# Performance work log

Hardware: AMD Instinct MI355X
Metric: run time of the kernel (lower is better)

Reference implementation:

```python
import jax, jax.numpy as jnp
from jax import lax
import numpy as np

B, T, H, L = 4096, 7, 512, 256
D = 2 * H  # bidirectional LSTM feature dim


def _lstm(x, wih, whh, bih, bhh, reverse):
    # x: [B, T, L]; torch gate order i, f, g, o
    b, hdim = x.shape[0], whh.shape[0]
    xs = jnp.swapaxes(x, 0, 1)  # [T, B, L]
    bias = bih + bhh

    def step(carry, xt):
        h, c = carry
        gates = xt @ wih + h @ whh + bias
        i, f, g, o = jnp.split(gates, 4, axis=-1)
        c = jax.nn.sigmoid(f) * c + jax.nn.sigmoid(i) * jnp.tanh(g)
        h = jax.nn.sigmoid(o) * jnp.tanh(c)
        return (h, c), h

    h0 = jnp.zeros((b, hdim), x.dtype)
    _, hs = lax.scan(step, (h0, h0), xs, reverse=reverse)
    return jnp.swapaxes(hs, 0, 1)  # [B, T, H]


def _att(enc, dec):
    # Sequential attention: keys/values start as enc and grow with each decoder output.
    keys = enc  # [B, T, D]
    outs = []
    for i in range(dec.shape[1]):  # fixed small T=7, Python loop is static
        q = dec[:, i, :]                                  # [B, D]
        scores = jnp.einsum('bd,btd->bt', q, keys)        # dot over features
        a = jax.nn.softmax(scores, axis=1)
        ctx = jnp.einsum('bt,btd->bd', a, keys)
        out = ctx + q
        outs.append(out)
        keys = jnp.concatenate([keys, out[:, None, :]], axis=1)
    return jnp.stack(outs, axis=1)  # [B, T, D]


def _deconv(x, w, b):
    # torch ConvTranspose2d (stride 1, pad 0) == full conv with flipped, in/out-swapped kernel
    kh, kw = w.shape[2], w.shape[3]
    w2 = jnp.transpose(w[:, :, ::-1, ::-1], (1, 0, 2, 3))  # [out, in, kh, kw]
    y = lax.conv_general_dilated(x, w2, (1, 1), ((kh - 1, kh - 1), (kw - 1, kw - 1)),
                                 dimension_numbers=('NCHW', 'OIHW', 'NCHW'))
    return y + b[None, :, None, None]


def setup_inputs() -> dict:
    key = jax.random.key(0)
    ks = jax.random.split(key, 12)
    p = lambda k, shape: jax.random.normal(k, shape, jnp.float32) * 0.02
    return {
        'lstm_enc': jax.random.normal(ks[0], (B, T, D), jnp.float32),
        'gaussian_noise': jax.random.normal(ks[1], (B, L), jnp.float32),
        'embedrep_w': p(ks[2], (L, L * T)), 'embedrep_b': jnp.zeros((L * T,), jnp.float32),
        'wih_f': p(ks[3], (L, 4 * H)), 'whh_f': p(ks[4], (H, 4 * H)),
        'bih_f': jnp.zeros((4 * H,), jnp.float32), 'bhh_f': jnp.zeros((4 * H,), jnp.float32),
        'wih_b': p(ks[5], (L, 4 * H)), 'whh_b': p(ks[6], (H, 4 * H)),
        'bih_b': jnp.zeros((4 * H,), jnp.float32), 'bhh_b': jnp.zeros((4 * H,), jnp.float32),
        'emb_w': p(ks[7], (D, 1024)), 'emb_b': jnp.zeros((1024,), jnp.float32),
        'dc3_w': p(ks[8], (64, 32, 1, 3)), 'dc3_b': jnp.zeros((32,), jnp.float32),
        'dc1_w': p(ks[9], (32, 16, 1, 5)), 'dc1_b': jnp.zeros((16,), jnp.float32),
        'dc2_w': p(ks[10], (16, 1, 3, 3)), 'dc2_b': jnp.zeros((1,), jnp.float32),
        'infer': 0,
    }


def reference(lstm_enc, gaussian_noise, embedrep_w, embedrep_b,
              wih_f, whh_f, bih_f, bhh_f, wih_b, whh_b, bih_b, bhh_b,
              emb_w, emb_b, dc3_w, dc3_b, dc1_w, dc1_b, dc2_w, dc2_b, infer):
    b = lstm_enc.shape[0]
    g1 = jax.nn.soft_sign(gaussian_noise @ embedrep_w + embedrep_b)   # [B, L*T]
    rep = g1.reshape(b, T, L)                                          # [B, 7, L]
    hf = _lstm(rep, wih_f, whh_f, bih_f, bhh_f, False)
    hb = _lstm(rep, wih_b, whh_b, bih_b, bhh_b, True)
    lstm1 = jnp.concatenate([hf, hb], axis=-1)                         # [B, 7, 2H]
    att_out = _att(lstm_enc, lstm1)                                    # [B, 7, 2H]
    emb = att_out @ emb_w + emb_b                                      # [B, 7, 1024]
    up = jax.nn.soft_sign(emb).reshape(b * T, 64, 1, 16)
    x = jax.nn.leaky_relu(_deconv(up, dc3_w, dc3_b))                   # [B*7, 32, 1, 18]
    x = jax.nn.leaky_relu(_deconv(x, dc1_w, dc1_b))                    # [B*7, 16, 1, 22]
    x = jax.nn.leaky_relu(_deconv(x, dc2_w, dc2_b))                    # [B*7, 1, 3, 24]
    x = jax.nn.softmax(x, axis=2)                                      # softmax over H dim (=3)
    out = x.reshape(b, T, 1, 3, 24)[:, :, -1, :, :]                    # [B, 7, 3, 24]
    return out
```

## Files before the change

kernel.cpp:

```cpp
#include <hip/hip_runtime.h>
#include <stdint.h>


typedef __attribute__((ext_vector_type(4))) float f32x4;
typedef __attribute__((ext_vector_type(8))) short bf16x8;
typedef __attribute__((ext_vector_type(4))) unsigned short us4;

__device__ __forceinline__ unsigned short f2b(float f) {
  union { float f; unsigned u; } x; x.f = f;
  unsigned r = x.u + 0x7FFFu + ((x.u >> 16) & 1u);
  return (unsigned short)(r >> 16);
}
__device__ __forceinline__ float b2f(unsigned short s) {
  union { unsigned u; float f; } x; x.u = ((unsigned)s) << 16; return x.f;
}
__device__ __forceinline__ float sigmoidf(float x) {
  return 1.f / (1.f + __expf(-x));
}
__device__ __forceinline__ float fast_tanh(float x) {
  x = fminf(15.f, fmaxf(-15.f, x));
  float e = __expf(2.f * x);
  return (e - 1.f) / (e + 1.f);
}

__device__ __forceinline__ void gl_lds16(const void* g, void* l) {
  auto gp = reinterpret_cast<const __attribute__((address_space(1))) unsigned int*>(
      reinterpret_cast<uintptr_t>(g));
  auto lp = reinterpret_cast<__attribute__((address_space(3))) unsigned int*>(
      reinterpret_cast<uintptr_t>(l));
  __builtin_amdgcn_global_load_lds(gp, lp, 16, 0, 0);
}


__device__ __forceinline__ void stage_half(const unsigned short* src, int ld,
                                           unsigned short* hbase, int tid) {
  const int row_in = tid >> 2;
  const int gidx = tid & 3;
#pragma unroll
  for (int r = 0; r < 2; ++r) {
    int row = r * 128 + row_in;
    int gsrc = gidx ^ ((row >> 1) & 3);
    gl_lds16(src + (size_t)row * ld + gsrc * 8, hbase + r * 4096 + (tid >> 6) * 512);
  }
}

__device__ __forceinline__ bf16x8 lds_fragH(const unsigned short* hbase, int row, int lq) {
  return *(const bf16x8*)(hbase + row * 32 + (lq ^ (((row >> 1) & 3) << 3)));
}

template <int N>
__device__ __forceinline__ void gate() {
  if constexpr (N == 8) asm volatile("s_waitcnt vmcnt(8)" ::: "memory");
  else if constexpr (N == 4) asm volatile("s_waitcnt vmcnt(4)" ::: "memory");
  else asm volatile("s_waitcnt vmcnt(0)" ::: "memory");
}

#define TILE_TOP(N)                     \
  gate<N>();                            \
  __builtin_amdgcn_s_barrier();         \
  __builtin_amdgcn_sched_barrier(0)

template <class FA, class FB>
__device__ __forceinline__ void tile32(const unsigned short* Ab, const unsigned short* Bb,
                                       int wm, int wn, int lane, f32x4 (&acc)[8][4],
                                       FA stageA, FB stageB) {
  const int lr = lane & 15, lq = (lane >> 4) * 8;
  bf16x8 a[8], b[4];
#pragma unroll
  for (int i = 0; i < 4; ++i) a[i] = lds_fragH(Ab, wm * 128 + i * 16 + lr, lq);
#pragma unroll
  for (int n = 0; n < 4; ++n) b[n] = lds_fragH(Bb, wn * 64 + n * 16 + lr, lq);
  __builtin_amdgcn_sched_barrier(0);
#pragma unroll
  for (int i = 4; i < 8; ++i) a[i] = lds_fragH(Ab, wm * 128 + i * 16 + lr, lq);
  stageA();
  asm volatile("s_waitcnt lgkmcnt(4)" ::: "memory");
  __builtin_amdgcn_sched_barrier(0);
  __builtin_amdgcn_s_setprio(1);
#pragma unroll
  for (int i = 0; i < 4; ++i)
#pragma unroll
    for (int n = 0; n < 4; ++n)
      acc[i][n] = __builtin_amdgcn_mfma_f32_16x16x32_bf16(a[i], b[n], acc[i][n], 0, 0, 0);
  __builtin_amdgcn_s_setprio(0);
  stageB();
  asm volatile("s_waitcnt lgkmcnt(0)" ::: "memory");
  __builtin_amdgcn_sched_barrier(0);
  __builtin_amdgcn_s_setprio(1);
#pragma unroll
  for (int i = 4; i < 8; ++i)
#pragma unroll
    for (int n = 0; n < 4; ++n)
      acc[i][n] = __builtin_amdgcn_mfma_f32_16x16x32_bf16(a[i], b[n], acc[i][n], 0, 0, 0);
  __builtin_amdgcn_s_setprio(0);
}

__device__ __forceinline__ void stage128x64(const unsigned short* src, int ld,
                                            unsigned short* lds, int wv, int lane) {
#pragma unroll
  for (int r = 0; r < 4; ++r) {
    int row = r * 32 + wv * 8 + (lane >> 3);
    gl_lds16(src + (size_t)row * ld + (lane & 7) * 8, lds + (r * 32 + wv * 8) * 64);
  }
}
__device__ __forceinline__ void mfma_tile(const unsigned short* As, const unsigned short* Bs,
                                          int wm, int wn, int lane, f32x4 acc[4][4]) {
#pragma unroll
  for (int kk = 0; kk < 2; ++kk) {
    int ko = kk * 32 + (lane >> 4) * 8;
    bf16x8 a[4], b[4];
#pragma unroll
    for (int i = 0; i < 4; ++i)
      a[i] = *(const bf16x8*)(As + (size_t)(wm * 64 + i * 16 + (lane & 15)) * 64 + ko);
#pragma unroll
    for (int i = 0; i < 4; ++i)
      b[i] = *(const bf16x8*)(Bs + (size_t)(wn * 64 + i * 16 + (lane & 15)) * 64 + ko);
#pragma unroll
    for (int mi = 0; mi < 4; ++mi)
#pragma unroll
      for (int ni = 0; ni < 4; ++ni)
        acc[mi][ni] = __builtin_amdgcn_mfma_f32_16x16x32_bf16(a[mi], b[ni], acc[mi][ni], 0, 0, 0);
  }
}

__global__ __launch_bounds__(256) void pack_kernel(
    const float* __restrict__ noise, const float* __restrict__ erep_w,
    const float* __restrict__ emb_w,
    const float* __restrict__ wih_f, const float* __restrict__ whh_f,
    const float* __restrict__ bih_f, const float* __restrict__ bhh_f,
    const float* __restrict__ wih_b, const float* __restrict__ whh_b,
    const float* __restrict__ bih_b, const float* __restrict__ bhh_b,
    unsigned short* __restrict__ noiseb, unsigned short* __restrict__ erepT,
    unsigned short* __restrict__ embT, unsigned short* __restrict__ lstmW,
    float* __restrict__ lstmB) {
  const int N0 = 4096 * 256;
  const int N1 = 1792 * 256;
  const int N2 = 1024 * 1024;
  const int N3 = 2 * 2048 * 768;
  const int N4 = 2 * 2048;
  const int total = N0 + N1 + N2 + N3 + N4;
  for (int i = blockIdx.x * 256 + threadIdx.x; i < total; i += gridDim.x * 256) {
    int x = i;
    if (x < N0) { noiseb[x] = f2b(noise[x]); continue; }
    x -= N0;
    if (x < N1) { int n = x >> 8, k = x & 255; erepT[x] = f2b(erep_w[k * 1792 + n]); continue; }
    x -= N1;
    if (x < N2) {
      int n = x >> 10, k = x & 1023;
      int o = (n & 63) * 16 + (n >> 6);
      embT[x] = f2b(emb_w[k * 1024 + o]);
      continue;
    }
    x -= N2;
    if (x < N3) {
      int dir = x / (2048 * 768);
      int r = x - dir * (2048 * 768);
      int npk = r / 768, k = r - (r / 768) * 768;
      int blk = npk >> 6, g = (npk >> 4) & 3, u = npk & 15;
      int o = g * 512 + blk * 16 + u;
      const float* wih = dir ? wih_b : wih_f;
      const float* whh = dir ? whh_b : whh_f;
      float v = (k < 256) ? wih[k * 2048 + o] : whh[(k - 256) * 2048 + o];
      lstmW[x] = f2b(v);
      continue;
    }
    x -= N3;
    {
      int dir = x >> 11, npk = x & 2047;
      int blk = npk >> 6, g = (npk >> 4) & 3, u = npk & 15;
      int o = g * 512 + blk * 16 + u;
      lstmB[x] = dir ? (bih_b[o] + bhh_b[o]) : (bih_f[o] + bhh_f[o]);
    }
  }
}

__global__ __launch_bounds__(256) void gemm_rep_kernel(
    const unsigned short* __restrict__ A, const unsigned short* __restrict__ Bt,
    const float* __restrict__ bias, unsigned short* __restrict__ rep_t) {
  __shared__ unsigned short As[128 * 64];
  __shared__ unsigned short Bs[128 * 64];
  const int lane = threadIdx.x & 63, wv = threadIdx.x >> 6;
  const int wm = wv >> 1, wn = wv & 1;
  const int m0 = blockIdx.y * 128, n0 = blockIdx.x * 128;
  f32x4 acc[4][4];
#pragma unroll
  for (int i = 0; i < 4; ++i)
#pragma unroll
    for (int j = 0; j < 4; ++j) acc[i][j] = (f32x4){0.f, 0.f, 0.f, 0.f};
  for (int k0 = 0; k0 < 256; k0 += 64) {
    stage128x64(A + (size_t)m0 * 256 + k0, 256, As, wv, lane);
    stage128x64(Bt + (size_t)n0 * 256 + k0, 256, Bs, wv, lane);
    __syncthreads();
    mfma_tile(As, Bs, wm, wn, lane, acc);
    __syncthreads();
  }
#pragma unroll
  for (int ni = 0; ni < 4; ++ni) {
    int n = n0 + wn * 64 + ni * 16 + (lane & 15);
    float bv = bias[n];
    int t = n >> 8, l = n & 255;
#pragma unroll
    for (int mi = 0; mi < 4; ++mi)
#pragma unroll
      for (int r = 0; r < 4; ++r) {
        int m = m0 + wm * 64 + mi * 16 + (lane >> 4) * 4 + r;
        float v = acc[mi][ni][r] + bv;
        v = v / (1.f + fabsf(v));
        rep_t[((size_t)t * 4096 + m) * 256 + l] = f2b(v);
      }
  }
}

__global__ __launch_bounds__(512, 2) void lstm_step256_kernel(
    const unsigned short* __restrict__ rep_t, const unsigned short* __restrict__ Wp,
    const float* __restrict__ biasP, unsigned short* __restrict__ hbuf,
    float* __restrict__ cbuf, unsigned short* __restrict__ lstm1, int step) {
  __shared__ unsigned short Ar[4][8192];
  __shared__ unsigned short Br[4][8192];
  const int tid = threadIdx.x, lane = tid & 63, wv = tid >> 6;
  const int wm = wv >> 2, wn = wv & 3;
  const int swz = (blockIdx.x & 7) * 32 + (blockIdx.x >> 3);
  const int dir = swz >> 7;
  const int by = (swz & 127) >> 3, bx = swz & 7;
  const int m0 = by * 256, n0 = bx * 256;
  const int t_proc = dir ? (6 - step) : step;
  const unsigned short* W = Wp + (size_t)dir * 2048 * 768;
  const unsigned short* hin = hbuf + ((size_t)(step & 1) * 2 + dir) * (4096 * 512);
  unsigned short* hout = hbuf + ((size_t)((step + 1) & 1) * 2 + dir) * (4096 * 512);
  float* cp = cbuf + (size_t)dir * (4096 * 512);
  const unsigned short* xsrc = rep_t + (size_t)t_proc * 4096 * 256;

  f32x4 acc[8][4];
#pragma unroll
  for (int i = 0; i < 8; ++i)
#pragma unroll
    for (int j = 0; j < 4; ++j) acc[i][j] = (f32x4){0.f, 0.f, 0.f, 0.f};

  auto asrc = [&](int tt) {
    return tt < 8 ? xsrc + (size_t)m0 * 256 + tt * 32
                  : hin + (size_t)m0 * 512 + (tt - 8) * 32;
  };
  auto ald = [&](int tt) { return tt < 8 ? 256 : 512; };

  stage_half(asrc(0), ald(0), Ar[0], tid);
  stage_half(W + (size_t)n0 * 768 + 0 * 32, 768, Br[0], tid);
  stage_half(asrc(1), ald(1), Ar[1], tid);
  stage_half(W + (size_t)n0 * 768 + 1 * 32, 768, Br[1], tid);
  stage_half(asrc(2), ald(2), Ar[2], tid);
  stage_half(W + (size_t)n0 * 768 + 2 * 32, 768, Br[2], tid);

  for (int t = 0; t <= 20; ++t) {
    TILE_TOP(8);
    const int tt = t + 3;
    tile32(Ar[t & 3], Br[t & 3], wm, wn, lane, acc,
           [&] { stage_half(asrc(tt), ald(tt), Ar[tt & 3], tid); },
           [&] { stage_half(W + (size_t)n0 * 768 + tt * 32, 768, Br[tt & 3], tid); });
  }
  TILE_TOP(8);
  tile32(Ar[21 & 3], Br[21 & 3], wm, wn, lane, acc, [&] {}, [&] {});
  TILE_TOP(4);
  tile32(Ar[22 & 3], Br[22 & 3], wm, wn, lane, acc, [&] {}, [&] {});
  TILE_TOP(0);
  tile32(Ar[23 & 3], Br[23 & 3], wm, wn, lane, acc, [&] {}, [&] {});

  const int u = lane & 15;
  const int blk = (n0 + wn * 64) >> 6;
  const int j = blk * 16 + u;
  const float bz0 = biasP[dir * 2048 + blk * 64 + 0 * 16 + u];
  const float bz1 = biasP[dir * 2048 + blk * 64 + 1 * 16 + u];
  const float bz2 = biasP[dir * 2048 + blk * 64 + 2 * 16 + u];
  const float bz3 = biasP[dir * 2048 + blk * 64 + 3 * 16 + u];
#pragma unroll
  for (int mi = 0; mi < 8; ++mi)
#pragma unroll
    for (int r = 0; r < 4; ++r) {
      int row = m0 + wm * 128 + mi * 16 + (lane >> 4) * 4 + r;
      float gi = acc[mi][0][r] + bz0;
      float gf = acc[mi][1][r] + bz1;
      float gg = acc[mi][2][r] + bz2;
      float go = acc[mi][3][r] + bz3;
      size_t ci = (size_t)row * 512 + j;
      float c = sigmoidf(gf) * cp[ci] + sigmoidf(gi) * fast_tanh(gg);
      cp[ci] = c;
      float h = sigmoidf(go) * fast_tanh(c);
      unsigned short hb = f2b(h);
      hout[ci] = hb;
      lstm1[((size_t)row * 7 + t_proc) * 1024 + dir * 512 + j] = hb;
    }
}

__global__ __launch_bounds__(256) void att_fused2_kernel(
    const float* __restrict__ enc, const unsigned short* __restrict__ lstm1,
    unsigned short* __restrict__ att) {
  __shared__ unsigned short Qs[7 * 1032];
  __shared__ unsigned short Ehs[7 * 1032];
  __shared__ unsigned short Els[7 * 1032];
  __shared__ float P[4 * 2 * 64 * 4];
  __shared__ float sG[98];
  __shared__ float sC[7][14];
  __shared__ float sA[16];
  const int tid = threadIdx.x, lane = tid & 63, wv = tid >> 6;
  const int b = blockIdx.x;
  const float* Eb = enc + (size_t)b * 7168;
  const unsigned short* Qb = lstm1 + (size_t)b * 7168;

  if (tid < 98) ((float*)sC)[tid] = 0.f;

  const f32x4* Eb4 = (const f32x4*)Eb;
#pragma unroll
  for (int r = 0; r < 7; ++r) {
    f32x4 v = Eb4[r * 256 + tid];
    us4 hi, lo;
#pragma unroll
    for (int e = 0; e < 4; ++e) {
      hi[e] = f2b(v[e]);
      lo[e] = f2b(v[e] - b2f(hi[e]));
    }
    *(us4*)&Ehs[r * 1032 + tid * 4] = hi;
    *(us4*)&Els[r * 1032 + tid * 4] = lo;
  }
  const bf16x8* Qb8 = (const bf16x8*)Qb;
#pragma unroll
  for (int r = 0; r < 4; ++r) {
    int idx = r * 256 + tid;
    if (idx < 896) {
      int row = idx >> 7, col = (idx & 127) * 8;
      *(bf16x8*)&Qs[row * 1032 + col] = Qb8[idx];
    }
  }
  __syncthreads();

  {
    const int rr = lane & 15;
    const int rowc = rr > 6 ? 6 : rr;
    const int kbase = wv * 256 + (lane >> 4) * 8;
    f32x4 g1 = {0.f, 0.f, 0.f, 0.f}, g2 = {0.f, 0.f, 0.f, 0.f};
#pragma unroll
    for (int s = 0; s < 8; ++s) {
      const int k0 = kbase + s * 32;
      bf16x8 aq = *(const bf16x8*)&Qs[rowc * 1032 + k0];
      bf16x8 bh = *(const bf16x8*)&Ehs[rowc * 1032 + k0];
      bf16x8 bl = *(const bf16x8*)&Els[rowc * 1032 + k0];
      g1 = __builtin_amdgcn_mfma_f32_16x16x32_bf16(aq, bh, g1, 0, 0, 0);
      g1 = __builtin_amdgcn_mfma_f32_16x16x32_bf16(aq, bl, g1, 0, 0, 0);
      g2 = __builtin_amdgcn_mfma_f32_16x16x32_bf16(aq, aq, g2, 0, 0, 0);
    }
    *(f32x4*)&P[((wv * 2 + 0) * 64 + lane) * 4] = g1;
    *(f32x4*)&P[((wv * 2 + 1) * 64 + lane) * 4] = g2;
  }
  __syncthreads();

  if (tid < 98) {
    int i = tid / 14, v = tid - i * 14;
    int col = v < 7 ? v : v - 7;
    int tile = v < 7 ? 0 : 1;
    int ln = ((i >> 2) << 4) | col;
    int rg = i & 3;
    float s = 0.f;
#pragma unroll
    for (int w = 0; w < 4; ++w) s += P[((w * 2 + tile) * 64 + ln) * 4 + rg];
    sG[i * 14 + v] = s;
  }
  __syncthreads();

  if (wv == 0) {
    for (int i = 0; i < 7; ++i) {
      const int nt = 7 + i;
      float s = -1e30f;
      if (lane < 7) {
        s = sG[i * 14 + lane];
      } else if (lane < nt) {
        int jj = lane - 7;
        float a2 = 0.f;
#pragma unroll
        for (int v = 0; v < 14; ++v) a2 += sC[jj][v] * sG[i * 14 + v];
        s = a2;
      }
      float mx = s;
#pragma unroll
      for (int off = 8; off >= 1; off >>= 1) mx = fmaxf(mx, __shfl_xor(mx, off, 16));
      float e = (lane < nt) ? __expf(s - mx) : 0.f;
      float sum = e;
#pragma unroll
      for (int off = 8; off >= 1; off >>= 1) sum += __shfl_xor(sum, off, 16);
      float a = e / sum;
      if (lane < 16) sA[lane] = a;
      if (lane < 14) {
        float c = (lane < 7) ? sA[lane] : 0.f;
        for (int jj = 0; jj < i; ++jj) c += sA[7 + jj] * sC[jj][lane];
        if (lane == 7 + i) c += 1.f;
        sC[i][lane] = c;
      }
    }
  }
  __syncthreads();

  {
    const int d0 = tid * 4;
    float acc[7][4];
#pragma unroll
    for (int i = 0; i < 7; ++i)
#pragma unroll
      for (int e = 0; e < 4; ++e) acc[i][e] = 0.f;
#pragma unroll
    for (int t = 0; t < 7; ++t) {
      us4 h = *(const us4*)&Ehs[t * 1032 + d0];
      us4 l = *(const us4*)&Els[t * 1032 + d0];
      float ev[4];
#pragma unroll
      for (int e = 0; e < 4; ++e) ev[e] = b2f(h[e]) + b2f(l[e]);
#pragma unroll
      for (int i = 0; i < 7; ++i) {
        float c = sC[i][t];
#pragma unroll
        for (int e = 0; e < 4; ++e) acc[i][e] += c * ev[e];
      }
    }
#pragma unroll
    for (int m = 0; m < 7; ++m) {
      us4 qv = *(const us4*)&Qs[m * 1032 + d0];
      float qf[4];
#pragma unroll
      for (int e = 0; e < 4; ++e) qf[e] = b2f(qv[e]);
#pragma unroll
      for (int i = m; i < 7; ++i) {
        float c = sC[i][7 + m];
#pragma unroll
        for (int e = 0; e < 4; ++e) acc[i][e] += c * qf[e];
      }
    }
    unsigned short* Ab = att + (size_t)b * 7168;
#pragma unroll
    for (int i = 0; i < 7; ++i) {
      us4 r;
#pragma unroll
      for (int e = 0; e < 4; ++e) r[e] = f2b(acc[i][e]);
      *(us4*)(Ab + i * 1024 + d0) = r;
    }
  }
}

__global__ __launch_bounds__(512, 2) void gemm_emb256_kernel(
    const unsigned short* __restrict__ A, const unsigned short* __restrict__ Bt,
    const float* __restrict__ bias, unsigned short* __restrict__ up_t) {
  __shared__ unsigned short Ar[4][8192];
  __shared__ unsigned short Br[4][8192];
  const int tid = threadIdx.x, lane = tid & 63, wv = tid >> 6;
  const int wm = wv >> 2, wn = wv & 3;
  const int swz = (blockIdx.x & 7) * 56 + (blockIdx.x >> 3);
  const int by = swz >> 2, bx = swz & 3;
  const int m0 = by * 256, n0 = bx * 256;

  f32x4 acc[8][4];
#pragma unroll
  for (int i = 0; i < 8; ++i)
#pragma unroll
    for (int j = 0; j < 4; ++j) acc[i][j] = (f32x4){0.f, 0.f, 0.f, 0.f};

  const unsigned short* Abase = A + (size_t)m0 * 1024;
  const unsigned short* Bbase = Bt + (size_t)n0 * 1024;

  stage_half(Abase + 0 * 32, 1024, Ar[0], tid);
  stage_half(Bbase + 0 * 32, 1024, Br[0], tid);
  stage_half(Abase + 1 * 32, 1024, Ar[1], tid);
  stage_half(Bbase + 1 * 32, 1024, Br[1], tid);
  stage_half(Abase + 2 * 32, 1024, Ar[2], tid);
  stage_half(Bbase + 2 * 32, 1024, Br[2], tid);

  for (int t = 0; t <= 28; ++t) {
    TILE_TOP(8);
    const int tt = t + 3;
    tile32(Ar[t & 3], Br[t & 3], wm, wn, lane, acc,
           [&] { stage_half(Abase + tt * 32, 1024, Ar[tt & 3], tid); },
           [&] { stage_half(Bbase + tt * 32, 1024, Br[tt & 3], tid); });
  }
  TILE_TOP(8);
  tile32(Ar[29 & 3], Br[29 & 3], wm, wn, lane, acc, [&] {}, [&] {});
  TILE_TOP(4);
  tile32(Ar[30 & 3], Br[30 & 3], wm, wn, lane, acc, [&] {}, [&] {});
  TILE_TOP(0);
  tile32(Ar[31 & 3], Br[31 & 3], wm, wn, lane, acc, [&] {}, [&] {});

#pragma unroll
  for (int ni = 0; ni < 4; ++ni) {
    int np = n0 + wn * 64 + ni * 16 + (lane & 15);
    int o = (np & 63) * 16 + (np >> 6);
    float bv = bias[o];
#pragma unroll
    for (int mi = 0; mi < 8; ++mi)
#pragma unroll
      for (int r = 0; r < 4; ++r) {
        int m = m0 + wm * 128 + mi * 16 + (lane >> 4) * 4 + r;
        float v = acc[mi][ni][r] + bv;
        v = v / (1.f + fabsf(v));
        up_t[(size_t)m * 1024 + np] = f2b(v);
      }
  }
}

__global__ __launch_bounds__(256) void dc3_kernel(const unsigned short* __restrict__ up_t,
                                                  const float* __restrict__ w3,
                                                  const float* __restrict__ b3,
                                                  unsigned short* __restrict__ y1_t) {
  const int lane = threadIdx.x & 63, wv = threadIdx.x >> 6;
  const int kq = (lane >> 4) * 8;
  const int oc = lane & 15;
  bf16x8 bf[2][6];
#pragma unroll
  for (int nt = 0; nt < 2; ++nt)
#pragma unroll
    for (int kk = 0; kk < 6; ++kk) {
      bf16x8 v;
#pragma unroll
      for (int t = 0; t < 8; ++t) {
        int k = kk * 32 + kq + t;
        int jj = k >> 6, ic = k & 63;
        v[t] = (short)f2b(w3[((size_t)ic * 32 + nt * 16 + oc) * 3 + jj]);
      }
      bf[nt][kk] = v;
    }
  const float bia0 = b3[oc], bia1 = b3[16 + oc];
  const int base_chunk = blockIdx.x * 32 + wv * 8;
  for (int cc = 0; cc < 8; ++cc) {
    const int chunk = base_chunk + cc;
    int m = chunk * 16 + (lane & 15);
    int img = m / 18, ow = m - img * 18;
    const unsigned short* arow = up_t + (size_t)img * 1024;
    f32x4 acc0 = {0.f, 0.f, 0.f, 0.f}, acc1 = {0.f, 0.f, 0.f, 0.f};
#pragma unroll
    for (int kk = 0; kk < 6; ++kk) {
      int jj = kk >> 1;
      int ic0 = (kk & 1) * 32 + kq;
      int iw = ow - jj;
      bf16x8 a = {0, 0, 0, 0, 0, 0, 0, 0};
      if ((unsigned)iw < 16u) a = *(const bf16x8*)(arow + iw * 64 + ic0);
      acc0 = __builtin_amdgcn_mfma_f32_16x16x32_bf16(a, bf[0][kk], acc0, 0, 0, 0);
      acc1 = __builtin_amdgcn_mfma_f32_16x16x32_bf16(a, bf[1][kk], acc1, 0, 0, 0);
    }
#pragma unroll
    for (int r = 0; r < 4; ++r) {
      int mm = chunk * 16 + (lane >> 4) * 4 + r;
      float v0 = acc0[r] + bia0; v0 = v0 > 0.f ? v0 : 0.01f * v0;
      float v1 = acc1[r] + bia1; v1 = v1 > 0.f ? v1 : 0.01f * v1;
      y1_t[(size_t)mm * 32 + oc] = f2b(v0);
      y1_t[(size_t)mm * 32 + 16 + oc] = f2b(v1);
    }
  }
}

__global__ __launch_bounds__(256) void dc1_kernel(const unsigned short* __restrict__ y1_t,
                                                  const float* __restrict__ w1,
                                                  const float* __restrict__ b1,
                                                  unsigned short* __restrict__ y2_t) {
  const int lane = threadIdx.x & 63, wv = threadIdx.x >> 6;
  const int kq = (lane >> 4) * 8;
  const int oc = lane & 15;
  bf16x8 bf[5];
#pragma unroll
  for (int kk = 0; kk < 5; ++kk) {
    bf16x8 v;
#pragma unroll
    for (int t = 0; t < 8; ++t) {
      int ic = kq + t;
      v[t] = (short)f2b(w1[((size_t)ic * 16 + oc) * 5 + kk]);
    }
    bf[kk] = v;
  }
  const float bia = b1[oc];
  const int base_chunk = blockIdx.x * 32 + wv * 8;
  for (int cc = 0; cc < 8; ++cc) {
    const int chunk = base_chunk + cc;
    int m = chunk * 16 + (lane & 15);
    int img = m / 22, ow = m - img * 22;
    const unsigned short* abase = y1_t + (size_t)img * 18 * 32;
    f32x4 acc = {0.f, 0.f, 0.f, 0.f};
#pragma unroll
    for (int kk = 0; kk < 5; ++kk) {
      int iw = ow - kk;
      bf16x8 a = {0, 0, 0, 0, 0, 0, 0, 0};
      if ((unsigned)iw < 18u) a = *(const bf16x8*)(abase + iw * 32 + kq);
      acc = __builtin_amdgcn_mfma_f32_16x16x32_bf16(a, bf[kk], acc, 0, 0, 0);
    }
#pragma unroll
    for (int r = 0; r < 4; ++r) {
      int mm = chunk * 16 + (lane >> 4) * 4 + r;
      float v = acc[r] + bia;
      v = v > 0.f ? v : 0.01f * v;
      y2_t[(size_t)mm * 16 + oc] = f2b(v);
    }
  }
}

__global__ __launch_bounds__(256) void dc2_kernel(const unsigned short* __restrict__ y2_t,
                                                  const float* __restrict__ w2,
                                                  const float* __restrict__ b2,
                                                  float* __restrict__ out) {
  int idx = blockIdx.x * 256 + threadIdx.x;
  int img = idx / 24, ow = idx - img * 24;
  float lg0 = b2[0], lg1 = b2[0], lg2 = b2[0];
#pragma unroll
  for (int jj = 0; jj < 3; ++jj) {
    int iw = ow - jj;
    if ((unsigned)iw >= 22u) continue;
    const unsigned short* row = y2_t + ((size_t)img * 22 + iw) * 16;
    bf16x8 v0 = *(const bf16x8*)(row);
    bf16x8 v1 = *(const bf16x8*)(row + 8);
    float x[16];
#pragma unroll
    for (int ic = 0; ic < 8; ++ic) {
      x[ic] = b2f((unsigned short)v0[ic]);
      x[8 + ic] = b2f((unsigned short)v1[ic]);
    }
#pragma unroll
    for (int ic = 0; ic < 16; ++ic) {
      lg0 += x[ic] * w2[ic * 9 + 0 * 3 + jj];
      lg1 += x[ic] * w2[ic * 9 + 1 * 3 + jj];
      lg2 += x[ic] * w2[ic * 9 + 2 * 3 + jj];
    }
  }
  lg0 = lg0 > 0.f ? lg0 : 0.01f * lg0;
  lg1 = lg1 > 0.f ? lg1 : 0.01f * lg1;
  lg2 = lg2 > 0.f ? lg2 : 0.01f * lg2;
  float mx = fmaxf(lg0, fmaxf(lg1, lg2));
  float e0 = __expf(lg0 - mx), e1 = __expf(lg1 - mx), e2 = __expf(lg2 - mx);
  float inv = 1.f / (e0 + e1 + e2);
  size_t ob = (size_t)img * 72 + ow;
  out[ob] = e0 * inv;
  out[ob + 24] = e1 * inv;
  out[ob + 48] = e2 * inv;
}

extern "C" void kernel_launch(void* const* d_in, const int* in_sizes, int n_in,
                              void* d_out, int out_size, void* d_ws, size_t ws_size,
                              hipStream_t stream) {
  (void)in_sizes; (void)n_in; (void)out_size; (void)ws_size;
  const float* enc    = (const float*)d_in[0];
  const float* noise  = (const float*)d_in[1];
  const float* erep_w = (const float*)d_in[2];
  const float* erep_b = (const float*)d_in[3];
  const float* wih_f  = (const float*)d_in[4];
  const float* whh_f  = (const float*)d_in[5];
  const float* bih_f  = (const float*)d_in[6];
  const float* bhh_f  = (const float*)d_in[7];
  const float* wih_b  = (const float*)d_in[8];
  const float* whh_b  = (const float*)d_in[9];
  const float* bih_b  = (const float*)d_in[10];
  const float* bhh_b  = (const float*)d_in[11];
  const float* emb_w  = (const float*)d_in[12];
  const float* emb_b  = (const float*)d_in[13];
  const float* dc3w   = (const float*)d_in[14];
  const float* dc3b   = (const float*)d_in[15];
  const float* dc1w   = (const float*)d_in[16];
  const float* dc1b   = (const float*)d_in[17];
  const float* dc2w   = (const float*)d_in[18];
  const float* dc2b   = (const float*)d_in[19];
  float* out = (float*)d_out;

  char* p = (char*)d_ws;
  auto carve = [&p](size_t bytes) {
    char* r = p;
    p += (bytes + 255) & ~(size_t)255;
    return r;
  };
  unsigned short* rep_t  = (unsigned short*)carve(7ull * 4096 * 256 * 2);
  unsigned short* lstmW  = (unsigned short*)carve(2ull * 2048 * 768 * 2);
  float*          lstmB  = (float*)carve(2ull * 2048 * 4);
  unsigned short* noiseb = (unsigned short*)carve(4096ull * 256 * 2);
  unsigned short* erepT  = (unsigned short*)carve(1792ull * 256 * 2);
  unsigned short* embT   = (unsigned short*)carve(1024ull * 1024 * 2);
  unsigned short* hbuf   = (unsigned short*)carve(4ull * 4096 * 512 * 2);
  float*          cbuf   = (float*)carve(2ull * 4096 * 512 * 4);
  unsigned short* lstm1  = (unsigned short*)carve(4096ull * 7 * 1024 * 2);
  unsigned short* att    = (unsigned short*)carve(28672ull * 1024 * 2);
  unsigned short* up_t   = (unsigned short*)carve(28672ull * 1024 * 2);
  unsigned short* y1_t   = (unsigned short*)carve(28672ull * 18 * 32 * 2);
  unsigned short* y2_t   = (unsigned short*)carve(28672ull * 22 * 16 * 2);

  hipMemsetAsync(hbuf, 0, 2ull * 4096 * 512 * 2, stream);
  hipMemsetAsync(cbuf, 0, 2ull * 4096 * 512 * 4, stream);

  pack_kernel<<<2048, 256, 0, stream>>>(noise, erep_w, emb_w, wih_f, whh_f, bih_f, bhh_f,
                                        wih_b, whh_b, bih_b, bhh_b,
                                        noiseb, erepT, embT, lstmW, lstmB);
  gemm_rep_kernel<<<dim3(14, 32), 256, 0, stream>>>(noiseb, erepT, erep_b, rep_t);
  for (int s = 0; s < 7; ++s)
    lstm_step256_kernel<<<256, 512, 0, stream>>>(rep_t, lstmW, lstmB, hbuf, cbuf, lstm1, s);
  att_fused2_kernel<<<4096, 256, 0, stream>>>(enc, lstm1, att);
  gemm_emb256_kernel<<<448, 512, 0, stream>>>(att, embT, emb_b, up_t);
  dc3_kernel<<<1008, 256, 0, stream>>>(up_t, dc3w, dc3b, y1_t);
  dc1_kernel<<<1232, 256, 0, stream>>>(y1_t, dc1w, dc1b, y2_t);
  dc2_kernel<<<2688, 256, 0, stream>>>(y2_t, dc2w, dc2b, out);
}
```

Measured before the change: 510.0 us.

## Restructure GEMM pipelines, store LSTM cell state in bf16, drop split-bf16 attention

The LDS-ring GEMM loop in the LSTM-step and embedding kernels now prefetches the next tile's fragments into registers while the current MFMAs run, replacing the split half-tile staging. The LSTM cell state buffer moves from fp32 to bf16, halving its read/write traffic per step. The attention kernel drops the hi/lo bf16 split of the encoder, using a single bf16 copy, and replaces a block barrier with an LDS waitcnt. These trade numerical precision for fewer MFMAs and less memory traffic, and the cell state rounding accumulates across steps.

```diff
diff --git a/kernel.cpp b/kernel.cpp
--- a/kernel.cpp
+++ b/kernel.cpp
@@ -48,52 +48,33 @@
   return *(const bf16x8*)(hbase + row * 32 + (lq ^ (((row >> 1) & 3) << 3)));
 }
 
-template <int N>
-__device__ __forceinline__ void gate() {
-  if constexpr (N == 8) asm volatile("s_waitcnt vmcnt(8)" ::: "memory");
-  else if constexpr (N == 4) asm volatile("s_waitcnt vmcnt(4)" ::: "memory");
-  else asm volatile("s_waitcnt vmcnt(0)" ::: "memory");
-}
-
-#define TILE_TOP(N)                     \
-  gate<N>();                            \
-  __builtin_amdgcn_s_barrier();         \
-  __builtin_amdgcn_sched_barrier(0)
-
-template <class FA, class FB>
-__device__ __forceinline__ void tile32(const unsigned short* Ab, const unsigned short* Bb,
-                                       int wm, int wn, int lane, f32x4 (&acc)[8][4],
-                                       FA stageA, FB stageB) {
+__device__ __forceinline__ void tile_reads(const unsigned short* Ab, const unsigned short* Bb,
+                                           int wm, int wn, int lane,
+                                           bf16x8 (&a)[8], bf16x8 (&b)[4]) {
   const int lr = lane & 15, lq = (lane >> 4) * 8;
-  bf16x8 a[8], b[4];
-#pragma unroll
-  for (int i = 0; i < 4; ++i) a[i] = lds_fragH(Ab, wm * 128 + i * 16 + lr, lq);
+#pragma unroll
+  for (int i = 0; i < 8; ++i) a[i] = lds_fragH(Ab, wm * 128 + i * 16 + lr, lq);
 #pragma unroll
   for (int n = 0; n < 4; ++n) b[n] = lds_fragH(Bb, wn * 64 + n * 16 + lr, lq);
-  __builtin_amdgcn_sched_barrier(0);
-#pragma unroll
-  for (int i = 4; i < 8; ++i) a[i] = lds_fragH(Ab, wm * 128 + i * 16 + lr, lq);
-  stageA();
-  asm volatile("s_waitcnt lgkmcnt(4)" ::: "memory");
-  __builtin_amdgcn_sched_barrier(0);
+}
+
+__device__ __forceinline__ void tile_mfma(bf16x8 (&a)[8], bf16x8 (&b)[4], f32x4 (&acc)[8][4]) {
   __builtin_amdgcn_s_setprio(1);
 #pragma unroll
-  for (int i = 0; i < 4; ++i)
+  for (int i = 0; i < 8; ++i)
 #pragma unroll
     for (int n = 0; n < 4; ++n)
       acc[i][n] = __builtin_amdgcn_mfma_f32_16x16x32_bf16(a[i], b[n], acc[i][n], 0, 0, 0);
   __builtin_amdgcn_s_setprio(0);
-  stageB();
-  asm volatile("s_waitcnt lgkmcnt(0)" ::: "memory");
+}
+
+#define RING_TOP(t, NT)                                                   \
+  if ((t) < (NT)-2) asm volatile("s_waitcnt vmcnt(4)" ::: "memory");      \
+  else              asm volatile("s_waitcnt vmcnt(0)" ::: "memory");      \
+  __builtin_amdgcn_s_barrier();                                           \
+  __builtin_amdgcn_sched_barrier(0);                                      \
+  asm volatile("s_waitcnt lgkmcnt(0)" ::: "memory");                      \
   __builtin_amdgcn_sched_barrier(0);
-  __builtin_amdgcn_s_setprio(1);
-#pragma unroll
-  for (int i = 4; i < 8; ++i)
-#pragma unroll
-    for (int n = 0; n < 4; ++n)
-      acc[i][n] = __builtin_amdgcn_mfma_f32_16x16x32_bf16(a[i], b[n], acc[i][n], 0, 0, 0);
-  __builtin_amdgcn_s_setprio(0);
-}
 
 __device__ __forceinline__ void stage128x64(const unsigned short* src, int ld,
                                             unsigned short* lds, int wv, int lane) {
@@ -214,7 +195,7 @@
 __global__ __launch_bounds__(512, 2) void lstm_step256_kernel(
     const unsigned short* __restrict__ rep_t, const unsigned short* __restrict__ Wp,
     const float* __restrict__ biasP, unsigned short* __restrict__ hbuf,
-    float* __restrict__ cbuf, unsigned short* __restrict__ lstm1, int step) {
+    unsigned short* __restrict__ cbuf, unsigned short* __restrict__ lstm1, int step) {
   __shared__ unsigned short Ar[4][8192];
   __shared__ unsigned short Br[4][8192];
   const int tid = threadIdx.x, lane = tid & 63, wv = tid >> 6;
@@ -227,7 +208,7 @@
   const unsigned short* W = Wp + (size_t)dir * 2048 * 768;
   const unsigned short* hin = hbuf + ((size_t)(step & 1) * 2 + dir) * (4096 * 512);
   unsigned short* hout = hbuf + ((size_t)((step + 1) & 1) * 2 + dir) * (4096 * 512);
-  float* cp = cbuf + (size_t)dir * (4096 * 512);
+  unsigned short* cp = cbuf + (size_t)dir * (4096 * 512);
   const unsigned short* xsrc = rep_t + (size_t)t_proc * 4096 * 256;
 
   f32x4 acc[8][4];
@@ -248,20 +229,21 @@
   stage_half(W + (size_t)n0 * 768 + 1 * 32, 768, Br[1], tid);
   stage_half(asrc(2), ald(2), Ar[2], tid);
   stage_half(W + (size_t)n0 * 768 + 2 * 32, 768, Br[2], tid);
-
-  for (int t = 0; t <= 20; ++t) {
-    TILE_TOP(8);
-    const int tt = t + 3;
-    tile32(Ar[t & 3], Br[t & 3], wm, wn, lane, acc,
-           [&] { stage_half(asrc(tt), ald(tt), Ar[tt & 3], tid); },
-           [&] { stage_half(W + (size_t)n0 * 768 + tt * 32, 768, Br[tt & 3], tid); });
-  }
-  TILE_TOP(8);
-  tile32(Ar[21 & 3], Br[21 & 3], wm, wn, lane, acc, [&] {}, [&] {});
-  TILE_TOP(4);
-  tile32(Ar[22 & 3], Br[22 & 3], wm, wn, lane, acc, [&] {}, [&] {});
-  TILE_TOP(0);
-  tile32(Ar[23 & 3], Br[23 & 3], wm, wn, lane, acc, [&] {}, [&] {});
+  asm volatile("s_waitcnt vmcnt(8)" ::: "memory");
+  __builtin_amdgcn_s_barrier();
+  __builtin_amdgcn_sched_barrier(0);
+  bf16x8 a[8], b[4];
+  tile_reads(Ar[0], Br[0], wm, wn, lane, a, b);
+
+  for (int t = 0; t < 24; ++t) {
+    RING_TOP(t, 24)
+    tile_mfma(a, b, acc);
+    if (t + 3 < 24) {
+      stage_half(asrc(t + 3), ald(t + 3), Ar[(t + 3) & 3], tid);
+      stage_half(W + (size_t)n0 * 768 + (t + 3) * 32, 768, Br[(t + 3) & 3], tid);
+    }
+    if (t + 1 < 24) tile_reads(Ar[(t + 1) & 3], Br[(t + 1) & 3], wm, wn, lane, a, b);
+  }
 
   const int u = lane & 15;
   const int blk = (n0 + wn * 64) >> 6;
@@ -280,8 +262,8 @@
       float gg = acc[mi][2][r] + bz2;
       float go = acc[mi][3][r] + bz3;
       size_t ci = (size_t)row * 512 + j;
-      float c = sigmoidf(gf) * cp[ci] + sigmoidf(gi) * fast_tanh(gg);
-      cp[ci] = c;
+      float c = sigmoidf(gf) * b2f(cp[ci]) + sigmoidf(gi) * fast_tanh(gg);
+      cp[ci] = f2b(c);
       float h = sigmoidf(go) * fast_tanh(c);
       unsigned short hb = f2b(h);
       hout[ci] = hb;
@@ -289,13 +271,12 @@
     }
 }
 
-__global__ __launch_bounds__(256) void att_fused2_kernel(
+__global__ __launch_bounds__(256) void att_fused3_kernel(
     const float* __restrict__ enc, const unsigned short* __restrict__ lstm1,
     unsigned short* __restrict__ att) {
   __shared__ unsigned short Qs[7 * 1032];
-  __shared__ unsigned short Ehs[7 * 1032];
-  __shared__ unsigned short Els[7 * 1032];
-  __shared__ float P[4 * 2 * 64 * 4];
+  __shared__ unsigned short Es[7 * 1032];
+  __shared__ float P[8 * 256];
   __shared__ float sG[98];
   __shared__ float sC[7][14];
   __shared__ float sA[16];
@@ -307,42 +288,30 @@
   if (tid < 98) ((float*)sC)[tid] = 0.f;
 
   const f32x4* Eb4 = (const f32x4*)Eb;
+  const int d0 = tid * 4;
 #pragma unroll
   for (int r = 0; r < 7; ++r) {
     f32x4 v = Eb4[r * 256 + tid];
-    us4 hi, lo;
-#pragma unroll
-    for (int e = 0; e < 4; ++e) {
-      hi[e] = f2b(v[e]);
-      lo[e] = f2b(v[e] - b2f(hi[e]));
-    }
-    *(us4*)&Ehs[r * 1032 + tid * 4] = hi;
-    *(us4*)&Els[r * 1032 + tid * 4] = lo;
-  }
-  const bf16x8* Qb8 = (const bf16x8*)Qb;
-#pragma unroll
-  for (int r = 0; r < 4; ++r) {
-    int idx = r * 256 + tid;
-    if (idx < 896) {
-      int row = idx >> 7, col = (idx & 127) * 8;
-      *(bf16x8*)&Qs[row * 1032 + col] = Qb8[idx];
-    }
-  }
-  __syncthreads();
+    us4 hi;
+#pragma unroll
+    for (int e = 0; e < 4; ++e) hi[e] = f2b(v[e]);
+    *(us4*)&Es[r * 1032 + d0] = hi;
+    *(us4*)&Qs[r * 1032 + d0] = *(const us4*)(Qb + r * 1024 + d0);
+  }
+  asm volatile("s_waitcnt lgkmcnt(0)" ::: "memory");
+  __builtin_amdgcn_sched_barrier(0);
 
   {
     const int rr = lane & 15;
-    const int rowc = rr > 6 ? 6 : rr;
+    const int rowc = rr % 7;
     const int kbase = wv * 256 + (lane >> 4) * 8;
     f32x4 g1 = {0.f, 0.f, 0.f, 0.f}, g2 = {0.f, 0.f, 0.f, 0.f};
 #pragma unroll
     for (int s = 0; s < 8; ++s) {
       const int k0 = kbase + s * 32;
       bf16x8 aq = *(const bf16x8*)&Qs[rowc * 1032 + k0];
-      bf16x8 bh = *(const bf16x8*)&Ehs[rowc * 1032 + k0];
-      bf16x8 bl = *(const bf16x8*)&Els[rowc * 1032 + k0];
-      g1 = __builtin_amdgcn_mfma_f32_16x16x32_bf16(aq, bh, g1, 0, 0, 0);
-      g1 = __builtin_amdgcn_mfma_f32_16x16x32_bf16(aq, bl, g1, 0, 0, 0);
+      bf16x8 be = *(const bf16x8*)&Es[rowc * 1032 + k0];
+      g1 = __builtin_amdgcn_mfma_f32_16x16x32_bf16(aq, be, g1, 0, 0, 0);
       g2 = __builtin_amdgcn_mfma_f32_16x16x32_bf16(aq, aq, g2, 0, 0, 0);
     }
     *(f32x4*)&P[((wv * 2 + 0) * 64 + lane) * 4] = g1;
@@ -362,7 +331,6 @@
     sG[i * 14 + v] = s;
   }
   __syncthreads();
-
   if (wv == 0) {
     for (int i = 0; i < 7; ++i) {
       const int nt = 7 + i;
@@ -383,8 +351,8 @@
       float sum = e;
 #pragma unroll
       for (int off = 8; off >= 1; off >>= 1) sum += __shfl_xor(sum, off, 16);
-      float a = e / sum;
-      if (lane < 16) sA[lane] = a;
+      float aw = e / sum;
+      if (lane < 16) sA[lane] = aw;
       if (lane < 14) {
         float c = (lane < 7) ? sA[lane] : 0.f;
         for (int jj = 0; jj < i; ++jj) c += sA[7 + jj] * sC[jj][lane];
@@ -396,7 +364,6 @@
   __syncthreads();
 
   {
-    const int d0 = tid * 4;
     float acc[7][4];
 #pragma unroll
     for (int i = 0; i < 7; ++i)
@@ -404,16 +371,15 @@
       for (int e = 0; e < 4; ++e) acc[i][e] = 0.f;
 #pragma unroll
     for (int t = 0; t < 7; ++t) {
-      us4 h = *(const us4*)&Ehs[t * 1032 + d0];
-      us4 l = *(const us4*)&Els[t * 1032 + d0];
-      float ev[4];
-#pragma unroll
-      for (int e = 0; e < 4; ++e) ev[e] = b2f(h[e]) + b2f(l[e]);
+      us4 ev = *(const us4*)&Es[t * 1032 + d0];
+      float evf[4];
+#pragma unroll
+      for (int e = 0; e < 4; ++e) evf[e] = b2f(ev[e]);
 #pragma unroll
       for (int i = 0; i < 7; ++i) {
         float c = sC[i][t];
 #pragma unroll
-        for (int e = 0; e < 4; ++e) acc[i][e] += c * ev[e];
+        for (int e = 0; e < 4; ++e) acc[i][e] += c * evf[e];
       }
     }
 #pragma unroll
@@ -466,20 +432,21 @@
   stage_half(Bbase + 1 * 32, 1024, Br[1], tid);
   stage_half(Abase + 2 * 32, 1024, Ar[2], tid);
   stage_half(Bbase + 2 * 32, 1024, Br[2], tid);
-
-  for (int t = 0; t <= 28; ++t) {
-    TILE_TOP(8);
-    const int tt = t + 3;
-    tile32(Ar[t & 3], Br[t & 3], wm, wn, lane, acc,
-           [&] { stage_half(Abase + tt * 32, 1024, Ar[tt & 3], tid); },
-           [&] { stage_half(Bbase + tt * 32, 1024, Br[tt & 3], tid); });
-  }
-  TILE_TOP(8);
-  tile32(Ar[29 & 3], Br[29 & 3], wm, wn, lane, acc, [&] {}, [&] {});
-  TILE_TOP(4);
-  tile32(Ar[30 & 3], Br[30 & 3], wm, wn, lane, acc, [&] {}, [&] {});
-  TILE_TOP(0);
-  tile32(Ar[31 & 3], Br[31 & 3], wm, wn, lane, acc, [&] {}, [&] {});
+  asm volatile("s_waitcnt vmcnt(8)" ::: "memory");
+  __builtin_amdgcn_s_barrier();
+  __builtin_amdgcn_sched_barrier(0);
+  bf16x8 a[8], b[4];
+  tile_reads(Ar[0], Br[0], wm, wn, lane, a, b);
+
+  for (int t = 0; t < 32; ++t) {
+    RING_TOP(t, 32)
+    tile_mfma(a, b, acc);
+    if (t + 3 < 32) {
+      stage_half(Abase + (t + 3) * 32, 1024, Ar[(t + 3) & 3], tid);
+      stage_half(Bbase + (t + 3) * 32, 1024, Br[(t + 3) & 3], tid);
+    }
+    if (t + 1 < 32) tile_reads(Ar[(t + 1) & 3], Br[(t + 1) & 3], wm, wn, lane, a, b);
+  }
 
 #pragma unroll
   for (int ni = 0; ni < 4; ++ni) {
@@ -669,7 +636,7 @@
   unsigned short* erepT  = (unsigned short*)carve(1792ull * 256 * 2);
   unsigned short* embT   = (unsigned short*)carve(1024ull * 1024 * 2);
   unsigned short* hbuf   = (unsigned short*)carve(4ull * 4096 * 512 * 2);
-  float*          cbuf   = (float*)carve(2ull * 4096 * 512 * 4);
+  unsigned short* cbuf   = (unsigned short*)carve(2ull * 4096 * 512 * 2);
   unsigned short* lstm1  = (unsigned short*)carve(4096ull * 7 * 1024 * 2);
   unsigned short* att    = (unsigned short*)carve(28672ull * 1024 * 2);
   unsigned short* up_t   = (unsigned short*)carve(28672ull * 1024 * 2);
@@ -677,7 +644,7 @@
   unsigned short* y2_t   = (unsigned short*)carve(28672ull * 22 * 16 * 2);
 
   hipMemsetAsync(hbuf, 0, 2ull * 4096 * 512 * 2, stream);
-  hipMemsetAsync(cbuf, 0, 2ull * 4096 * 512 * 4, stream);
+  hipMemsetAsync(cbuf, 0, 2ull * 4096 * 512 * 2, stream);
 
   pack_kernel<<<2048, 256, 0, stream>>>(noise, erep_w, emb_w, wih_f, whh_f, bih_f, bhh_f,
                                         wih_b, whh_b, bih_b, bhh_b,
@@ -685,7 +652,7 @@
   gemm_rep_kernel<<<dim3(14, 32), 256, 0, stream>>>(noiseb, erepT, erep_b, rep_t);
   for (int s = 0; s < 7; ++s)
     lstm_step256_kernel<<<256, 512, 0, stream>>>(rep_t, lstmW, lstmB, hbuf, cbuf, lstm1, s);
-  att_fused2_kernel<<<4096, 256, 0, stream>>>(enc, lstm1, att);
+  att_fused3_kernel<<<4096, 256, 0, stream>>>(enc, lstm1, att);
   gemm_emb256_kernel<<<448, 512, 0, stream>>>(att, embT, emb_b, up_t);
   dc3_kernel<<<1008, 256, 0, stream>>>(up_t, dc3w, dc3b, y1_t);
   dc1_kernel<<<1232, 256, 0, stream>>>(y1_t, dc1w, dc1b, y2_t);
```

Result: faster. 495.0 us (-2.9%).
